# Optimization experiments

Measured on AMD Instinct MI355X. Metric: run time of the kernel, lower is better.

The kernel has to match this reference:

```python
import jax, jax.numpy as jnp
import numpy as np

BITS = 4
NIBBLES_PER_INT32 = 8  # 32 // 4
K, N, GROUP = 4096, 4096, 128
TOKENS = 8192


def setup_inputs() -> dict:
    key = jax.random.key(0)
    kx, kw, kz, ks = jax.random.split(key, 4)
    x = jax.random.normal(kx, (TOKENS, K), dtype=jnp.float32)
    # packed 4-bit weights: 8 nibbles per int32 word along the K axis
    qweight = jax.random.randint(kw, (K // NIBBLES_PER_INT32, N), jnp.iinfo(jnp.int32).min, jnp.iinfo(jnp.int32).max, dtype=jnp.int32)
    # packed 4-bit zero points: 8 nibbles per int32 word along the N axis
    G = K // GROUP
    qzeros = jax.random.randint(kz, (G, N // NIBBLES_PER_INT32), jnp.iinfo(jnp.int32).min, jnp.iinfo(jnp.int32).max, dtype=jnp.int32)
    # per-group scales (positive)
    scales = jax.random.uniform(ks, (G, N), dtype=jnp.float32, minval=0.001, maxval=0.02)
    g_idx = (jnp.arange(K, dtype=jnp.int32) // GROUP).astype(jnp.int32)
    return {"x": x, "qweight": qweight, "qzeros": qzeros, "scales": scales, "g_idx": g_idx}


def _unpack_rows(packed):
    # packed: [K//8, N] int32 -> [K, N] int32 nibbles (packed along rows)
    shifts = jnp.arange(NIBBLES_PER_INT32, dtype=jnp.int32) * BITS  # [8]
    nib = (packed[:, None, :] >> shifts[None, :, None]) & 0xF       # [K//8, 8, N]
    return nib.reshape(-1, packed.shape[1])                          # [K, N]


def _unpack_cols(packed):
    # packed: [G, N//8] int32 -> [G, N] int32 nibbles (packed along cols)
    shifts = jnp.arange(NIBBLES_PER_INT32, dtype=jnp.int32) * BITS  # [8]
    nib = (packed[:, :, None] >> shifts[None, None, :]) & 0xF       # [G, N//8, 8]
    return nib.reshape(packed.shape[0], -1)                          # [G, N]


def reference(x, qweight, qzeros, scales, g_idx):
    # GPTQ-style dequant: W[k, n] = (int_w[k, n] - z[g_idx[k], n]) * s[g_idx[k], n]
    w_int = _unpack_rows(qweight)                 # [K, N] in [0, 15]
    z_int = _unpack_cols(qzeros)                  # [G, N] in [0, 15]
    z = z_int[g_idx]                              # [K, N]
    s = scales[g_idx]                             # [K, N]
    W = (w_int - z).astype(scales.dtype) * s      # [K, N] dequantized
    return x @ W                                  # [TOKENS, N]
```

## Files before the change

### kernel.cpp

```cpp
#include <hip/hip_runtime.h>
#include <stdint.h>

#define M_DIM 8192
#define K_DIM 4096
#define N_DIM 4096

typedef int   i32x4 __attribute__((ext_vector_type(4)));
typedef float f32x4 __attribute__((ext_vector_type(4)));

__device__ __forceinline__ void gload16(const void* g, void* l) {
    __builtin_amdgcn_global_load_lds(
        (const __attribute__((address_space(1))) void*)g,
        (__attribute__((address_space(3))) void*)l,
        16, 0, 0);
}

__global__ __launch_bounds__(256) void conv_x_i8(const float* __restrict__ x,
                                                 int* __restrict__ xq,
                                                 float* __restrict__ xs) {
    int m = blockIdx.x, tid = threadIdx.x;
    const float* row = x + (size_t)m * K_DIM;
    float4 v[4];
    float mx = 0.f;
    #pragma unroll
    for (int i = 0; i < 4; ++i) {
        v[i] = *(const float4*)(row + i * 1024 + tid * 4);
        mx = fmaxf(mx, fmaxf(fmaxf(fabsf(v[i].x), fabsf(v[i].y)),
                             fmaxf(fabsf(v[i].z), fabsf(v[i].w))));
    }
    #pragma unroll
    for (int o = 32; o > 0; o >>= 1) mx = fmaxf(mx, __shfl_xor(mx, o, 64));
    __shared__ float red[4];
    if ((tid & 63) == 0) red[tid >> 6] = mx;
    __syncthreads();
    mx = fmaxf(fmaxf(red[0], red[1]), fmaxf(red[2], red[3]));
    mx = fmaxf(mx, 1e-20f);
    float inv = 127.f / mx;
    if (tid == 0) xs[m] = mx * (1.f / 127.f);
    #pragma unroll
    for (int i = 0; i < 4; ++i) {
        int q0 = (int)__builtin_rintf(v[i].x * inv);
        int q1 = (int)__builtin_rintf(v[i].y * inv);
        int q2 = (int)__builtin_rintf(v[i].z * inv);
        int q3 = (int)__builtin_rintf(v[i].w * inv);
        uint32_t p = (uint32_t)(q0 & 255) | ((uint32_t)(q1 & 255) << 8) |
                     ((uint32_t)(q2 & 255) << 16) | ((uint32_t)q3 << 24);
        xq[(size_t)m * (K_DIM / 4) + i * 256 + tid] = (int)p;
    }
}

#define DLROW 272
__global__ __launch_bounds__(256) void dequant_i8(const uint32_t* __restrict__ qw,
                                                  const uint32_t* __restrict__ qz,
                                                  const int* __restrict__ gidx,
                                                  signed char* __restrict__ wt) {
    __shared__ __align__(16) unsigned char lds[64 * DLROW];
    int tid = threadIdx.x;
    int n0  = blockIdx.x * 64;
    int k80 = blockIdx.y * 32;

    #pragma unroll
    for (int i = 0; i < 8; ++i) {
        int idx = i * 256 + tid;
        int k8l = idx >> 6;
        int nl  = idx & 63;
        int k8  = k80 + k8l;
        int nn  = n0 + nl;
        uint32_t w = qw[(size_t)k8 * N_DIM + nn];
        int g = gidx[k8 * 8];
        uint32_t zw = qz[(size_t)g * (N_DIM / 8) + (nn >> 3)];
        int z = (int)((zw >> ((nn & 7) * 4)) & 0xFu);
        uint64_t o = 0;
        #pragma unroll
        for (int j = 0; j < 8; ++j) {
            int wv = (int)((w >> (4 * j)) & 0xFu);
            o |= (uint64_t)(uint8_t)(signed char)(wv - z) << (8 * j);
        }
        *(uint64_t*)&lds[nl * DLROW + k8l * 8] = o;
    }
    __syncthreads();
    #pragma unroll
    for (int i = 0; i < 4; ++i) {
        int idx = i * 256 + tid;
        int row = idx >> 4;
        int c   = idx & 15;
        i32x4 v = *(const i32x4*)&lds[row * DLROW + c * 16];
        *(i32x4*)&wt[(size_t)(n0 + row) * K_DIM + k80 * 8 + c * 16] = v;
    }
}

__global__ __launch_bounds__(256, 2) void gemm_i8(const signed char* __restrict__ A,
                                                  const signed char* __restrict__ B,
                                                  const float* __restrict__ S,
                                                  const float* __restrict__ XS,
                                                  float* __restrict__ C) {
    __shared__ __align__(16) signed char As[128 * 128];
    __shared__ __align__(16) signed char Bs[128 * 128];
    __shared__ __align__(16) float Ss[128];

    int tid  = threadIdx.x;
    int lane = tid & 63;
    int wid  = tid >> 6;
    int l15  = lane & 15;
    int quad = lane >> 4;
    int wave_m = wid >> 1;
    int wave_n = wid & 1;

    int bm = blockIdx.y * 128;
    int bn = blockIdx.x * 128;

    int srow   = tid >> 3;
    int gchunk = (tid & 7) ^ (srow & 7);
    const signed char* gA = A + (size_t)(bm + srow) * K_DIM + gchunk * 16;
    const signed char* gB = B + (size_t)(bn + srow) * K_DIM + gchunk * 16;

    f32x4 facc[4][4];
    #pragma unroll
    for (int i = 0; i < 4; ++i)
        #pragma unroll
        for (int j = 0; j < 4; ++j)
            facc[i][j] = (f32x4){0.f, 0.f, 0.f, 0.f};

    const i32x4 zi = (i32x4){0, 0, 0, 0};
    int h = l15 & 7;

    for (int kt = 0; kt < K_DIM; kt += 128) {
        __syncthreads();
        #pragma unroll
        for (int i = 0; i < 4; ++i) {
            gload16(gA + kt + (size_t)i * 32 * K_DIM, As + i * 4096 + wid * 1024);
            gload16(gB + kt + (size_t)i * 32 * K_DIM, Bs + i * 4096 + wid * 1024);
        }
        if (tid < 32)
            gload16(S + ((size_t)(kt >> 7) * N_DIM + bn + tid * 4), Ss);
        asm volatile("s_waitcnt vmcnt(0)" ::: "memory");
        __syncthreads();

        float sv[4];
        #pragma unroll
        for (int nt = 0; nt < 4; ++nt)
            sv[nt] = Ss[wave_n * 64 + nt * 16 + l15];

        i32x4 bf[4][2];
        #pragma unroll
        for (int nt = 0; nt < 4; ++nt) {
            int brow = wave_n * 64 + nt * 16 + l15;
            bf[nt][0] = *(const i32x4*)&Bs[brow * 128 + ((quad) ^ h) * 16];
            bf[nt][1] = *(const i32x4*)&Bs[brow * 128 + ((4 + quad) ^ h) * 16];
        }

        #pragma unroll
        for (int mt = 0; mt < 4; ++mt) {
            int arow = wave_m * 64 + mt * 16 + l15;
            i32x4 a0 = *(const i32x4*)&As[arow * 128 + ((quad) ^ h) * 16];
            i32x4 a1 = *(const i32x4*)&As[arow * 128 + ((4 + quad) ^ h) * 16];
            #pragma unroll
            for (int nt = 0; nt < 4; ++nt) {
                i32x4 iacc = __builtin_amdgcn_mfma_i32_16x16x64_i8(a0, bf[nt][0], zi, 0, 0, 0);
                iacc = __builtin_amdgcn_mfma_i32_16x16x64_i8(a1, bf[nt][1], iacc, 0, 0, 0);
                #pragma unroll
                for (int r = 0; r < 4; ++r)
                    facc[mt][nt][r] += (float)iacc[r] * sv[nt];
            }
        }
    }

    #pragma unroll
    for (int mt = 0; mt < 4; ++mt) {
        int row0 = bm + wave_m * 64 + mt * 16 + quad * 4;
        float4 xsv = *(const float4*)(XS + row0);
        #pragma unroll
        for (int nt = 0; nt < 4; ++nt) {
            int col = bn + wave_n * 64 + nt * 16 + l15;
            C[(size_t)(row0 + 0) * N_DIM + col] = facc[mt][nt][0] * xsv.x;
            C[(size_t)(row0 + 1) * N_DIM + col] = facc[mt][nt][1] * xsv.y;
            C[(size_t)(row0 + 2) * N_DIM + col] = facc[mt][nt][2] * xsv.z;
            C[(size_t)(row0 + 3) * N_DIM + col] = facc[mt][nt][3] * xsv.w;
        }
    }
}

extern "C" void kernel_launch(void* const* d_in, const int* in_sizes, int n_in,
                              void* d_out, int out_size, void* d_ws, size_t ws_size,
                              hipStream_t stream) {
    const float*    x    = (const float*)d_in[0];
    const uint32_t* qw   = (const uint32_t*)d_in[1];
    const uint32_t* qz   = (const uint32_t*)d_in[2];
    const float*    sc   = (const float*)d_in[3];
    const int*      gidx = (const int*)d_in[4];
    float* out = (float*)d_out;

    signed char* xq = (signed char*)d_ws;
    signed char* wt = xq + (size_t)M_DIM * K_DIM;
    float*       xs = (float*)(wt + (size_t)N_DIM * K_DIM);

    conv_x_i8<<<dim3(M_DIM), 256, 0, stream>>>(x, (int*)xq, xs);
    dequant_i8<<<dim3(N_DIM / 64, K_DIM / 256), 256, 0, stream>>>(qw, qz, gidx, wt);
    gemm_i8<<<dim3(N_DIM / 128, M_DIM / 128), 256, 0, stream>>>(xq, wt, sc, xs, out);
}
```

Measured before the change: 388.8 us.

## Restructure int8 GEMM into 256x256 tiles with double-buffered phased pipeline

The int8 GEMM moves from 128x128 tiles with 4 waves to 256x256 tiles with 8 waves. A and B fragments are double-buffered in LDS, and each K-step is split into eight phases that interleave global-to-LDS prefetch of the next tile with MFMA work, using fine-grained vmcnt waits, s_setprio, and a swizzled 1D block order for L2 locality. The goal is to hide global load latency and raise arithmetic intensity per block. In exchange it uses much more LDS (about 128KB per block), which can cut occupancy, and the hand-tuned wait counts are fragile.

```diff
diff --git a/kernel.cpp b/kernel.cpp
--- a/kernel.cpp
+++ b/kernel.cpp
@@ -89,93 +89,154 @@
     }
 }
 
-__global__ __launch_bounds__(256, 2) void gemm_i8(const signed char* __restrict__ A,
+#define VMW(n) asm volatile("s_waitcnt vmcnt(" #n ")" ::: "memory")
+
+#define STAGE_A(bufi, t, s, j)                                                   \
+    gload16(ga + ((size_t)((s) * 64 + (j) * 128) * K_DIM + (size_t)(t) * 128),   \
+            &As[bufi][((((s) * 64 + (j) * 128 + sr)) << 7) + sc * 16])
+
+#define STAGE_B(bufi, t, s, j)                                                   \
+    gload16(gb + ((size_t)((s) * 32 + (j) * 128) * K_DIM + (size_t)(t) * 128),   \
+            &Bs[bufi][((((s) * 32 + (j) * 128 + brl)) << 7) + sc * 16])
+
+#define STAGE_S(bufi, t)                                                         \
+    gload16(S + (size_t)(t) * N_DIM + bn + lane * 4, &Sl[bufi][lane * 4])
+
+#define PHASE(bufi, mq, nq, STG, TAIL) do {                                      \
+    i32x4 af_[4][2], bf_[2][2];                                                  \
+    float sv0_ = Sl[bufi][wave_n * 64 + (nq) * 32 + l15];                        \
+    float sv1_ = Sl[bufi][wave_n * 64 + (nq) * 32 + 16 + l15];                   \
+    _Pragma("unroll")                                                            \
+    for (int m4_ = 0; m4_ < 4; ++m4_) {                                          \
+        const signed char* p_ =                                                  \
+            &As[bufi][(wave_m * 128 + ((mq) * 4 + m4_) * 16 + l15) << 7];        \
+        af_[m4_][0] = *(const i32x4*)(p_ + c0);                                  \
+        af_[m4_][1] = *(const i32x4*)(p_ + c1);                                  \
+    }                                                                            \
+    _Pragma("unroll")                                                            \
+    for (int n2_ = 0; n2_ < 2; ++n2_) {                                          \
+        const signed char* p_ =                                                  \
+            &Bs[bufi][(wave_n * 64 + ((nq) * 2 + n2_) * 16 + l15) << 7];         \
+        bf_[n2_][0] = *(const i32x4*)(p_ + c0);                                  \
+        bf_[n2_][1] = *(const i32x4*)(p_ + c1);                                  \
+    }                                                                            \
+    STG;                                                                         \
+    __builtin_amdgcn_s_barrier();                                                \
+    asm volatile("s_waitcnt lgkmcnt(0)" ::: "memory");                           \
+    __builtin_amdgcn_s_setprio(1);                                               \
+    _Pragma("unroll")                                                            \
+    for (int m4_ = 0; m4_ < 4; ++m4_) {                                          \
+        _Pragma("unroll")                                                        \
+        for (int n2_ = 0; n2_ < 2; ++n2_) {                                      \
+            i32x4 t0_ = __builtin_amdgcn_mfma_i32_16x16x64_i8(                   \
+                af_[m4_][0], bf_[n2_][0], (i32x4){0, 0, 0, 0}, 0, 0, 0);         \
+            i32x4 t1_ = __builtin_amdgcn_mfma_i32_16x16x64_i8(                   \
+                af_[m4_][1], bf_[n2_][1], t0_, 0, 0, 0);                         \
+            float ss_ = (n2_ ? sv1_ : sv0_);                                     \
+            _Pragma("unroll")                                                    \
+            for (int r_ = 0; r_ < 4; ++r_)                                       \
+                facc[(mq) * 4 + m4_][(nq) * 2 + n2_][r_] += (float)t1_[r_] * ss_;\
+        }                                                                        \
+    }                                                                            \
+    __builtin_amdgcn_s_setprio(0);                                               \
+    TAIL;                                                                        \
+    __builtin_amdgcn_s_barrier();                                                \
+    __builtin_amdgcn_sched_barrier(0);                                           \
+} while (0)
+
+__global__ __launch_bounds__(512, 2) void gemm_i8(const signed char* __restrict__ A,
                                                   const signed char* __restrict__ B,
                                                   const float* __restrict__ S,
                                                   const float* __restrict__ XS,
                                                   float* __restrict__ C) {
-    __shared__ __align__(16) signed char As[128 * 128];
-    __shared__ __align__(16) signed char Bs[128 * 128];
-    __shared__ __align__(16) float Ss[128];
-
-    int tid  = threadIdx.x;
-    int lane = tid & 63;
-    int wid  = tid >> 6;
-    int l15  = lane & 15;
-    int quad = lane >> 4;
-    int wave_m = wid >> 1;
-    int wave_n = wid & 1;
-
-    int bm = blockIdx.y * 128;
-    int bn = blockIdx.x * 128;
-
-    int srow   = tid >> 3;
-    int gchunk = (tid & 7) ^ (srow & 7);
-    const signed char* gA = A + (size_t)(bm + srow) * K_DIM + gchunk * 16;
-    const signed char* gB = B + (size_t)(bn + srow) * K_DIM + gchunk * 16;
-
-    f32x4 facc[4][4];
-    #pragma unroll
-    for (int i = 0; i < 4; ++i)
+    __shared__ __align__(16) signed char As[2][256 * 128];
+    __shared__ __align__(16) signed char Bs[2][256 * 128];
+    __shared__ __align__(16) float Sl[2][256];
+
+    const int tid  = threadIdx.x;
+    const int lane = tid & 63;
+    const int wid  = tid >> 6;
+    const int l15  = lane & 15;
+    const int quad = lane >> 4;
+    const int wave_m = wid >> 2;
+    const int wave_n = wid & 3;
+    const int h  = l15 & 7;
+    const int c0 = (quad ^ h) * 16;
+    const int c1 = ((4 + quad) ^ h) * 16;
+
+    int bid = blockIdx.x;
+    int swz = (bid & 7) * 64 + (bid >> 3);
+    int bm = (swz >> 4) * 256;
+    int bn = (swz & 15) * 256;
+
+    const int sr  = tid >> 3;
+    const int sc  = tid & 7;
+    const int gch = sc ^ (sr & 7);
+    const int brl = (sr & 31) + ((sr >> 5) << 6);
+    const signed char* ga = A + (size_t)(bm + sr) * K_DIM + gch * 16;
+    const signed char* gb = B + (size_t)(bn + brl) * K_DIM + gch * 16;
+
+    f32x4 facc[8][4];
+    #pragma unroll
+    for (int i = 0; i < 8; ++i)
         #pragma unroll
         for (int j = 0; j < 4; ++j)
             facc[i][j] = (f32x4){0.f, 0.f, 0.f, 0.f};
 
-    const i32x4 zi = (i32x4){0, 0, 0, 0};
-    int h = l15 & 7;
-
-    for (int kt = 0; kt < K_DIM; kt += 128) {
-        __syncthreads();
-        #pragma unroll
-        for (int i = 0; i < 4; ++i) {
-            gload16(gA + kt + (size_t)i * 32 * K_DIM, As + i * 4096 + wid * 1024);
-            gload16(gB + kt + (size_t)i * 32 * K_DIM, Bs + i * 4096 + wid * 1024);
-        }
-        if (tid < 32)
-            gload16(S + ((size_t)(kt >> 7) * N_DIM + bn + tid * 4), Ss);
-        asm volatile("s_waitcnt vmcnt(0)" ::: "memory");
-        __syncthreads();
-
-        float sv[4];
-        #pragma unroll
-        for (int nt = 0; nt < 4; ++nt)
-            sv[nt] = Ss[wave_n * 64 + nt * 16 + l15];
-
-        i32x4 bf[4][2];
-        #pragma unroll
-        for (int nt = 0; nt < 4; ++nt) {
-            int brow = wave_n * 64 + nt * 16 + l15;
-            bf[nt][0] = *(const i32x4*)&Bs[brow * 128 + ((quad) ^ h) * 16];
-            bf[nt][1] = *(const i32x4*)&Bs[brow * 128 + ((4 + quad) ^ h) * 16];
-        }
-
-        #pragma unroll
-        for (int mt = 0; mt < 4; ++mt) {
-            int arow = wave_m * 64 + mt * 16 + l15;
-            i32x4 a0 = *(const i32x4*)&As[arow * 128 + ((quad) ^ h) * 16];
-            i32x4 a1 = *(const i32x4*)&As[arow * 128 + ((4 + quad) ^ h) * 16];
-            #pragma unroll
-            for (int nt = 0; nt < 4; ++nt) {
-                i32x4 iacc = __builtin_amdgcn_mfma_i32_16x16x64_i8(a0, bf[nt][0], zi, 0, 0, 0);
-                iacc = __builtin_amdgcn_mfma_i32_16x16x64_i8(a1, bf[nt][1], iacc, 0, 0, 0);
-                #pragma unroll
-                for (int r = 0; r < 4; ++r)
-                    facc[mt][nt][r] += (float)iacc[r] * sv[nt];
-            }
-        }
-    }
-
-    #pragma unroll
-    for (int mt = 0; mt < 4; ++mt) {
-        int row0 = bm + wave_m * 64 + mt * 16 + quad * 4;
+    STAGE_S(0, 0);
+    STAGE_A(0, 0, 0, 0); STAGE_A(0, 0, 0, 1);
+    STAGE_B(0, 0, 0, 0); STAGE_B(0, 0, 0, 1);
+    STAGE_A(0, 0, 1, 0); STAGE_A(0, 0, 1, 1);
+    STAGE_B(0, 0, 1, 0); STAGE_B(0, 0, 1, 1);
+    STAGE_A(1, 1, 0, 0); STAGE_A(1, 1, 0, 1);
+    STAGE_B(1, 1, 0, 0); STAGE_B(1, 1, 0, 1);
+    VMW(4);
+    __builtin_amdgcn_s_barrier();
+    __builtin_amdgcn_sched_barrier(0);
+
+    #pragma clang loop unroll(disable)
+    for (int it = 0; it < 16; ++it) {
+        const int t1k = 2 * it + 1;
+        const bool nl = (it < 15);
+
+        PHASE(0, 0, 0,
+              { STAGE_S(1, t1k); STAGE_A(1, t1k, 1, 0); STAGE_A(1, t1k, 1, 1); },
+              { VMW(7); });
+        PHASE(0, 0, 1,
+              { STAGE_B(1, t1k, 1, 0); STAGE_B(1, t1k, 1, 1); },
+              {});
+        PHASE(0, 1, 0,
+              { if (nl) { STAGE_A(0, t1k + 1, 0, 0); STAGE_A(0, t1k + 1, 0, 1); } },
+              {});
+        PHASE(0, 1, 1,
+              { if (nl) { STAGE_B(0, t1k + 1, 0, 0); STAGE_B(0, t1k + 1, 0, 1); } },
+              { if (nl) { VMW(8); } else { VMW(0); } });
+        PHASE(1, 0, 0,
+              { if (nl) { STAGE_S(0, t1k + 1);
+                          STAGE_A(0, t1k + 1, 1, 0); STAGE_A(0, t1k + 1, 1, 1); } },
+              { if (nl) { VMW(7); } });
+        PHASE(1, 0, 1,
+              { if (nl) { STAGE_B(0, t1k + 1, 1, 0); STAGE_B(0, t1k + 1, 1, 1); } },
+              {});
+        PHASE(1, 1, 0,
+              { if (nl) { STAGE_A(1, t1k + 2, 0, 0); STAGE_A(1, t1k + 2, 0, 1); } },
+              {});
+        PHASE(1, 1, 1,
+              { if (nl) { STAGE_B(1, t1k + 2, 0, 0); STAGE_B(1, t1k + 2, 0, 1); } },
+              { if (nl) { VMW(8); } });
+    }
+
+    #pragma unroll
+    for (int mf = 0; mf < 8; ++mf) {
+        int row0 = bm + wave_m * 128 + mf * 16 + quad * 4;
         float4 xsv = *(const float4*)(XS + row0);
         #pragma unroll
-        for (int nt = 0; nt < 4; ++nt) {
-            int col = bn + wave_n * 64 + nt * 16 + l15;
-            C[(size_t)(row0 + 0) * N_DIM + col] = facc[mt][nt][0] * xsv.x;
-            C[(size_t)(row0 + 1) * N_DIM + col] = facc[mt][nt][1] * xsv.y;
-            C[(size_t)(row0 + 2) * N_DIM + col] = facc[mt][nt][2] * xsv.z;
-            C[(size_t)(row0 + 3) * N_DIM + col] = facc[mt][nt][3] * xsv.w;
+        for (int nf = 0; nf < 4; ++nf) {
+            int col = bn + wave_n * 64 + nf * 16 + l15;
+            C[(size_t)(row0 + 0) * N_DIM + col] = facc[mf][nf][0] * xsv.x;
+            C[(size_t)(row0 + 1) * N_DIM + col] = facc[mf][nf][1] * xsv.y;
+            C[(size_t)(row0 + 2) * N_DIM + col] = facc[mf][nf][2] * xsv.z;
+            C[(size_t)(row0 + 3) * N_DIM + col] = facc[mf][nf][3] * xsv.w;
         }
     }
 }
@@ -196,5 +257,5 @@
 
     conv_x_i8<<<dim3(M_DIM), 256, 0, stream>>>(x, (int*)xq, xs);
     dequant_i8<<<dim3(N_DIM / 64, K_DIM / 256), 256, 0, stream>>>(qw, qz, gidx, wt);
-    gemm_i8<<<dim3(N_DIM / 128, M_DIM / 128), 256, 0, stream>>>(xq, wt, sc, xs, out);
-}
+    gemm_i8<<<dim3(512), dim3(512), 0, stream>>>(xq, wt, sc, xs, out);
+}
```

Measured after the change: 1.511 ms. +288.7%, slower.
